# Kernel optimization log

Measured on AMD Instinct MI355X. Metric: run time of the kernel, lower is better.

The kernel has to match this reference:

```python
import jax, jax.numpy as jnp
import numpy as np

DIM = 2048
H = 16        # num query heads
HK = 2        # num kv heads
D = DIM // H  # head_dim = 128
G = H // HK   # q heads per kv head = 8
SCALE = 1.0 / np.sqrt(D)


def setup_inputs() -> dict:
    key = jax.random.key(0)
    ks = jax.random.split(key, 9)
    xavier = lambda k, fi, fo: jax.random.uniform(k, (fi, fo), jnp.float32,
                                                  -np.sqrt(6.0 / (fi + fo)), np.sqrt(6.0 / (fi + fo)))
    return {
        "x": jax.random.normal(ks[0], (2, 2048, DIM), jnp.float32),
        "Wq": xavier(ks[1], DIM, H * D),  "bq": jnp.zeros((H * D,), jnp.float32),
        "Wk": xavier(ks[2], DIM, HK * D), "bk": jnp.zeros((HK * D,), jnp.float32),
        "Wv": xavier(ks[3], DIM, HK * D), "bv": jnp.zeros((HK * D,), jnp.float32),
        "Wo": xavier(ks[4], H * D, DIM),  "bo": jnp.zeros((DIM,), jnp.float32),
    }


def reference(x, Wq, bq, Wk, bk, Wv, bv, Wo, bo):
    B, T, C = x.shape
    # projections; q grouped as (kv_head, group) so repeat_interleave becomes a broadcast
    q = (x @ Wq + bq).reshape(B, T, HK, G, D)   # [B,T,Hk,G,D]
    k = (x @ Wk + bk).reshape(B, T, HK, D)      # [B,T,Hk,D]
    v = (x @ Wv + bv).reshape(B, T, HK, D)
    # scores: [B,Hk,G,Tq,Tk] — shared K broadcast across the G query heads per kv head
    scores = jnp.einsum('bqhgd,bshd->bhgqs', q, k) * SCALE
    scores = jnp.clip(scores, -100.0, 100.0)
    attn = jax.nn.softmax(scores, axis=-1)
    out = jnp.einsum('bhgqs,bshd->bqhgd', attn, v).reshape(B, T, H * D)
    return out @ Wo + bo
```

## Files before the change

kernel.cpp:

```cpp
#include <hip/hip_runtime.h>
#include <cstdint>

typedef __bf16 bf16x8 __attribute__((ext_vector_type(8)));
typedef float floatx4 __attribute__((ext_vector_type(4)));
typedef float floatx16 __attribute__((ext_vector_type(16)));
typedef unsigned short u16;
typedef unsigned int u32;

#define SCALE2 0.1275434297677098f
#define CLIP2  144.26950408889634f
#define DEFER  8.0f

__device__ __forceinline__ u16 f2bf(float f) {
  union { float f; u32 i; } v; v.f = f;
  u32 r = v.i + 0x7fffu + ((v.i >> 16) & 1u);
  return (u16)(r >> 16);
}

__device__ __forceinline__ u32 cvtpk(float lo, float hi) {
  u32 r;
  asm("v_cvt_pk_bf16_f32 %0, %1, %2" : "=v"(r) : "v"(lo), "v"(hi));
  return r;
}

__device__ __forceinline__ void gll16(const void* g, void* l) {
  __builtin_amdgcn_global_load_lds(
      (const __attribute__((address_space(1))) u32*)g,
      (__attribute__((address_space(3))) u32*)l, 16, 0, 0);
}

__global__ __launch_bounds__(256) void convert_bf16(
    const float* __restrict__ src, u16* __restrict__ dst, int n4) {
  int i = blockIdx.x * 256 + threadIdx.x;
  if (i >= n4) return;
  float4 v = ((const float4*)src)[i];
  ushort4 o;
  o.x = f2bf(v.x); o.y = f2bf(v.y); o.z = f2bf(v.z); o.w = f2bf(v.w);
  ((ushort4*)dst)[i] = o;
}

__global__ __launch_bounds__(256) void transpose_cat(
    const float* __restrict__ W0, const float* __restrict__ W1,
    const float* __restrict__ W2,
    int n1, int n2, int ld0, int ld1, int ld2, int K, u16* __restrict__ Bt) {
  __shared__ u16 tile[32][33];
  const int k0 = blockIdx.x * 32, n0 = blockIdx.y * 32;
  const float* src; int ld, nb;
  if (n0 < n1)      { src = W0; ld = ld0; nb = n0; }
  else if (n0 < n2) { src = W1; ld = ld1; nb = n0 - n1; }
  else              { src = W2; ld = ld2; nb = n0 - n2; }
  const int tx = threadIdx.x, ty = threadIdx.y;
#pragma unroll
  for (int i = 0; i < 4; i++) {
    int k = ty + i * 8;
    tile[k][tx] = f2bf(src[(size_t)(k0 + k) * ld + nb + tx]);
  }
  __syncthreads();
#pragma unroll
  for (int i = 0; i < 4; i++) {
    int n = ty + i * 8;
    Bt[(size_t)(n0 + n) * K + k0 + tx] = tile[tx][n];
  }
}

template <int EPI>
__global__ __launch_bounds__(256) void gemm_bt(
    const u16* __restrict__ A, const u16* __restrict__ Bt,
    const float* __restrict__ bias0, const float* __restrict__ bias1,
    const float* __restrict__ bias2,
    u16* __restrict__ out0, u16* __restrict__ out1, u16* __restrict__ out2,
    float* __restrict__ outf,
    int M, int N, int K) {
  __shared__ u16 As[2][128][32];
  __shared__ u16 Bs[2][128][32];
  const int tid  = threadIdx.x;
  const int w    = tid >> 6, L = tid & 63, ln = L & 15, quad = L >> 4;
  const int m0   = blockIdx.y * 128, n0 = blockIdx.x * 128;
  const int mw   = (w & 1) * 64, nw = (w >> 1) * 64;
  const int sr = w * 32 + (L >> 2), sc = (L & 3) * 8;
  const u16* ga = &A [(size_t)(m0 + sr) * K + sc];
  const u16* gb = &Bt[(size_t)(n0 + sr) * K + sc];
  floatx4 acc[4][4] = {};
  const int nk = K >> 5;

  gll16(ga, &As[0][w * 32][0]);
  gll16(ga + (size_t)16 * K, &As[0][w * 32 + 16][0]);
  gll16(gb, &Bs[0][w * 32][0]);
  gll16(gb + (size_t)16 * K, &Bs[0][w * 32 + 16][0]);

  for (int i = 0; i < nk; i++) {
    const int cur = i & 1;
    __syncthreads();
    if (i + 1 < nk) {
      const int kt = (i + 1) << 5;
      gll16(ga + kt, &As[cur ^ 1][w * 32][0]);
      gll16(ga + (size_t)16 * K + kt, &As[cur ^ 1][w * 32 + 16][0]);
      gll16(gb + kt, &Bs[cur ^ 1][w * 32][0]);
      gll16(gb + (size_t)16 * K + kt, &Bs[cur ^ 1][w * 32 + 16][0]);
    }
    bf16x8 af[4], bf[4];
#pragma unroll
    for (int mb = 0; mb < 4; mb++) af[mb] = *(const bf16x8*)&As[cur][mw + mb * 16 + ln][quad * 8];
#pragma unroll
    for (int nb = 0; nb < 4; nb++) bf[nb] = *(const bf16x8*)&Bs[cur][nw + nb * 16 + ln][quad * 8];
#pragma unroll
    for (int mb = 0; mb < 4; mb++)
#pragma unroll
      for (int nb = 0; nb < 4; nb++)
        acc[mb][nb] = __builtin_amdgcn_mfma_f32_16x16x32_bf16(af[mb], bf[nb], acc[mb][nb], 0, 0, 0);
  }

#pragma unroll
  for (int mb = 0; mb < 4; mb++) {
#pragma unroll
    for (int nb = 0; nb < 4; nb++) {
#pragma unroll
      for (int r = 0; r < 4; r++) {
        const int m = m0 + mw + mb * 16 + quad * 4 + r;
        const int n = n0 + nw + nb * 16 + ln;
        float v = acc[mb][nb][r];
        if constexpr (EPI == 0) {
          if (n < 2048) {
            v = (v + bias0[n]) * SCALE2;
            out0[(size_t)m * 2048 + n] = f2bf(v);
          } else if (n < 2304) {
            const int j = n - 2048;
            v += bias1[j];
            out1[(size_t)m * 256 + j] = f2bf(v);
          } else {
            const int j = n - 2304;
            v += bias2[j];
            const int b = m >> 11, t = m & 2047;
            out2[((size_t)(b * 256 + j)) * 2048 + t] = f2bf(v);
          }
        } else {
          v += bias0[n];
          outf[(size_t)m * (size_t)N + n] = v;
        }
      }
    }
  }
}

__global__ __launch_bounds__(256, 2) void attn_kernel(
    const u16* __restrict__ Q, const u16* __restrict__ K,
    const u16* __restrict__ Vt, u16* __restrict__ O) {
  __shared__ u16 Ksh[2][16 * 512];
  __shared__ u16 Vsh[2][16 * 512];
  const int tid = threadIdx.x;
  const int w = tid >> 6, L = tid & 63;
  const int ln = L & 31, hf = L >> 5;
  const int qt = blockIdx.x, h = blockIdx.y, b = blockIdx.z;
  const int hk = h >> 3;
  const size_t qrow0 = (size_t)b * 2048 + qt * 128 + w * 32;

  const u16* Kbase = K + (size_t)b * 2048 * 256 + hk * 128;
  const u16* Vbase = Vt + (size_t)(b * 2 + hk) * 128 * 2048;

  const u16* gK[4];
  const u16* gV[4];
#pragma unroll
  for (int j = 0; j < 4; j++) {
    const int fK = 4 * w + j, mb = fK >> 3, kc = fK & 7;
    gK[j] = Kbase + (size_t)(mb * 32 + ln) * 256 + kc * 16 + hf * 8;
    const int fV = 4 * w + j, db = fV >> 2, ks = fV & 3;
    gV[j] = Vbase + (size_t)(db * 32 + ln) * 2048 + ks * 16 + hf * 8;
  }

  bf16x8 qf[8];
#pragma unroll
  for (int kc = 0; kc < 8; kc++)
    qf[kc] = *(const bf16x8*)&Q[(qrow0 + ln) * 2048 + h * 128 + kc * 16 + hf * 8];

  floatx16 oT[4] = {};
  float mrow = -1e30f, lrow = 0.f;

  auto issue = [&](int tile, int bufi) {
#pragma unroll
    for (int j = 0; j < 4; j++) {
      gll16(gK[j] + (size_t)tile * 64 * 256, &Ksh[bufi][(4 * w + j) * 512]);
      gll16(gV[j] + (size_t)tile * 64,       &Vsh[bufi][(4 * w + j) * 512]);
    }
  };

  auto qkt = [&](floatx16 (&sf)[2], const u16* kb) {
#pragma unroll
    for (int r = 0; r < 16; r++) { sf[0][r] = 0.f; sf[1][r] = 0.f; }
#pragma unroll
    for (int kc = 0; kc < 8; kc++) {
#pragma unroll
      for (int mb = 0; mb < 2; mb++) {
        bf16x8 kf = *(const bf16x8*)&kb[(mb * 8 + kc) * 512 + L * 8];
        sf[mb] = __builtin_amdgcn_mfma_f32_32x32x16_bf16(kf, qf[kc], sf[mb], 0, 0, 0);
      }
    }
  };

  auto softmax = [&](floatx16 (&sf)[2]) {
#pragma unroll
    for (int mb = 0; mb < 2; mb++)
#pragma unroll
      for (int r = 0; r < 16; r++)
        sf[mb][r] = __builtin_amdgcn_fmed3f(sf[mb][r], -CLIP2, CLIP2);
    float t16[16];
#pragma unroll
    for (int r = 0; r < 16; r++) t16[r] = fmaxf(sf[0][r], sf[1][r]);
#pragma unroll
    for (int d = 8; d >= 1; d >>= 1)
#pragma unroll
      for (int r = 0; r < d; r++) t16[r] = fmaxf(t16[r], t16[r + d]);
    const float mx = fmaxf(t16[0], __shfl_xor(t16[0], 32));
    const bool need = __ballot(mx > mrow + DEFER) != 0;
    float mn = mrow, alpha = 1.f;
    if (need) {
      mn = fmaxf(mrow, mx);
      alpha = __builtin_amdgcn_exp2f(mrow - mn);
      mrow = mn;
    }
#pragma unroll
    for (int mb = 0; mb < 2; mb++)
#pragma unroll
      for (int r = 0; r < 16; r++)
        sf[mb][r] = __builtin_amdgcn_exp2f(sf[mb][r] - mn);
    float s16[16];
#pragma unroll
    for (int r = 0; r < 16; r++) s16[r] = sf[0][r] + sf[1][r];
#pragma unroll
    for (int d = 8; d >= 1; d >>= 1)
#pragma unroll
      for (int r = 0; r < d; r++) s16[r] += s16[r + d];
    const float s = s16[0] + __shfl_xor(s16[0], 32);
    if (need) {
      lrow = lrow * alpha + s;
#pragma unroll
      for (int db = 0; db < 4; db++)
#pragma unroll
        for (int r = 0; r < 16; r++) oT[db][r] *= alpha;
    } else {
      lrow += s;
    }
  };

  auto pv = [&](floatx16 (&sf)[2], const u16* vb) {
#pragma unroll
    for (int ks = 0; ks < 4; ks++) {
      const int mb = ks >> 1, s8 = (ks & 1) * 8;
      u32 cA0 = cvtpk(sf[mb][s8 + 0], sf[mb][s8 + 1]);
      u32 cA1 = cvtpk(sf[mb][s8 + 2], sf[mb][s8 + 3]);
      u32 cB0 = cvtpk(sf[mb][s8 + 4], sf[mb][s8 + 5]);
      u32 cB1 = cvtpk(sf[mb][s8 + 6], sf[mb][s8 + 7]);
      asm("v_permlane32_swap_b32 %0, %1" : "+v"(cA0), "+v"(cB0));
      asm("v_permlane32_swap_b32 %0, %1" : "+v"(cA1), "+v"(cB1));
      union { u32 u[4]; bf16x8 v; } pb;
      pb.u[0] = cA0; pb.u[1] = cA1; pb.u[2] = cB0; pb.u[3] = cB1;
#pragma unroll
      for (int db = 0; db < 4; db++) {
        bf16x8 vf = *(const bf16x8*)&vb[(db * 4 + ks) * 512 + L * 8];
        oT[db] = __builtin_amdgcn_mfma_f32_32x32x16_bf16(vf, pb.v, oT[db], 0, 0, 0);
      }
    }
  };

  floatx16 sfA[2], sfB[2];

  issue(0, 0);
  __syncthreads();
  issue(1, 1);
  qkt(sfA, &Ksh[0][0]);

  for (int t = 0; t < 32; t += 2) {
    softmax(sfA);
    __syncthreads();
    __builtin_amdgcn_s_setprio(1);
    qkt(sfB, &Ksh[1][0]);
    pv(sfA, &Vsh[0][0]);
    __builtin_amdgcn_s_setprio(0);
    __syncthreads();
    if (t + 2 < 32) issue(t + 2, 0);
    softmax(sfB);
    __syncthreads();
    __builtin_amdgcn_s_setprio(1);
    if (t + 2 < 32) qkt(sfA, &Ksh[0][0]);
    pv(sfB, &Vsh[1][0]);
    __builtin_amdgcn_s_setprio(0);
    __syncthreads();
    if (t + 3 < 32) issue(t + 3, 1);
  }

  const float inv = 1.f / lrow;
  u16* orow = O + (qrow0 + ln) * 2048 + h * 128;
#pragma unroll
  for (int db = 0; db < 4; db++) {
#pragma unroll
    for (int g = 0; g < 4; g++) {
      uint2 st;
      st.x = cvtpk(oT[db][g * 4 + 0] * inv, oT[db][g * 4 + 1] * inv);
      st.y = cvtpk(oT[db][g * 4 + 2] * inv, oT[db][g * 4 + 3] * inv);
      *(uint2*)&orow[db * 32 + g * 8 + hf * 4] = st;
    }
  }
}

extern "C" void kernel_launch(void* const* d_in, const int* in_sizes, int n_in,
                              void* d_out, int out_size, void* d_ws, size_t ws_size,
                              hipStream_t stream) {
  const float* x  = (const float*)d_in[0];
  const float* Wq = (const float*)d_in[1];
  const float* bq = (const float*)d_in[2];
  const float* Wk = (const float*)d_in[3];
  const float* bk = (const float*)d_in[4];
  const float* Wv = (const float*)d_in[5];
  const float* bv = (const float*)d_in[6];
  const float* Wo = (const float*)d_in[7];
  const float* bo = (const float*)d_in[8];
  float* out = (float*)d_out;

  char* ws = (char*)d_ws;
  u16* xb     = (u16*)(ws);
  u16* Ob     = (u16*)(ws);
  u16* Wqkv_t = (u16*)(ws + 16777216);
  u16* Wot    = (u16*)(ws + 27262976);
  u16* Qb     = (u16*)(ws + 35651584);
  u16* Kb     = (u16*)(ws + 52428800);
  u16* Vtb    = (u16*)(ws + 54525952);
  (void)in_sizes; (void)n_in; (void)out_size; (void)ws_size;

  convert_bf16<<<8192, 256, 0, stream>>>(x, xb, 2097152);

  transpose_cat<<<dim3(64, 80), dim3(32, 8), 0, stream>>>(
      Wq, Wk, Wv, 2048, 2304, 2048, 256, 256, 2048, Wqkv_t);
  transpose_cat<<<dim3(64, 64), dim3(32, 8), 0, stream>>>(
      Wo, Wo, Wo, 2048, 2048, 2048, 2048, 2048, 2048, Wot);

  gemm_bt<0><<<dim3(20, 32), 256, 0, stream>>>(
      xb, Wqkv_t, bq, bk, bv, Qb, Kb, Vtb, nullptr, 4096, 2560, 2048);

  attn_kernel<<<dim3(16, 16, 2), 256, 0, stream>>>(Qb, Kb, Vtb, Ob);

  gemm_bt<1><<<dim3(16, 32), 256, 0, stream>>>(
      Ob, Wot, bo, nullptr, nullptr, nullptr, nullptr, nullptr, out, 4096, 2048, 2048);
}
```

Baseline: 328.5 us.

## Halve attention KV tile to 32 keys and merge weight transposes into one launch

The attention kernel now processes 32 keys per tile instead of 64. This halves the K/V shared-memory buffers and the score registers, doubles the number of loop iterations, and simplifies the softmax reductions. The smaller footprint may allow more waves per CU or a better schedule, but it adds twice as many barriers and tile issues for the same total work. Separately, the two weight-transpose launches are merged into a single grid to save one kernel launch.

Result: no change. 332.2 us (+1.1%).

```diff
diff --git a/kernel.cpp b/kernel.cpp
--- a/kernel.cpp
+++ b/kernel.cpp
@@ -39,16 +39,21 @@
   ((ushort4*)dst)[i] = o;
 }
 
-__global__ __launch_bounds__(256) void transpose_cat(
-    const float* __restrict__ W0, const float* __restrict__ W1,
-    const float* __restrict__ W2,
-    int n1, int n2, int ld0, int ld1, int ld2, int K, u16* __restrict__ Bt) {
+__global__ __launch_bounds__(256) void transpose_all(
+    const float* __restrict__ Wq, const float* __restrict__ Wk,
+    const float* __restrict__ Wv, const float* __restrict__ Wo,
+    u16* __restrict__ Wqkv_t, u16* __restrict__ Wot) {
   __shared__ u16 tile[32][33];
-  const int k0 = blockIdx.x * 32, n0 = blockIdx.y * 32;
-  const float* src; int ld, nb;
-  if (n0 < n1)      { src = W0; ld = ld0; nb = n0; }
-  else if (n0 < n2) { src = W1; ld = ld1; nb = n0 - n1; }
-  else              { src = W2; ld = ld2; nb = n0 - n2; }
+  const int k0 = blockIdx.x * 32, ny = blockIdx.y;
+  const float* src; int ld, nb, n0; u16* dst;
+  if (ny < 80) {
+    n0 = ny * 32; dst = Wqkv_t;
+    if (n0 < 2048)      { src = Wq; ld = 2048; nb = n0; }
+    else if (n0 < 2304) { src = Wk; ld = 256;  nb = n0 - 2048; }
+    else                { src = Wv; ld = 256;  nb = n0 - 2304; }
+  } else {
+    n0 = (ny - 80) * 32; dst = Wot; src = Wo; ld = 2048; nb = n0;
+  }
   const int tx = threadIdx.x, ty = threadIdx.y;
 #pragma unroll
   for (int i = 0; i < 4; i++) {
@@ -59,7 +64,7 @@
 #pragma unroll
   for (int i = 0; i < 4; i++) {
     int n = ty + i * 8;
-    Bt[(size_t)(n0 + n) * K + k0 + tx] = tile[tx][n];
+    dst[(size_t)(n0 + n) * 2048 + k0 + tx] = tile[tx][n];
   }
 }
 
@@ -145,8 +150,8 @@
 __global__ __launch_bounds__(256, 2) void attn_kernel(
     const u16* __restrict__ Q, const u16* __restrict__ K,
     const u16* __restrict__ Vt, u16* __restrict__ O) {
-  __shared__ u16 Ksh[2][16 * 512];
-  __shared__ u16 Vsh[2][16 * 512];
+  __shared__ u16 Ksh[2][8 * 512];
+  __shared__ u16 Vsh[2][8 * 512];
   const int tid = threadIdx.x;
   const int w = tid >> 6, L = tid & 63;
   const int ln = L & 31, hf = L >> 5;
@@ -157,13 +162,13 @@
   const u16* Kbase = K + (size_t)b * 2048 * 256 + hk * 128;
   const u16* Vbase = Vt + (size_t)(b * 2 + hk) * 128 * 2048;
 
-  const u16* gK[4];
-  const u16* gV[4];
-#pragma unroll
-  for (int j = 0; j < 4; j++) {
-    const int fK = 4 * w + j, mb = fK >> 3, kc = fK & 7;
-    gK[j] = Kbase + (size_t)(mb * 32 + ln) * 256 + kc * 16 + hf * 8;
-    const int fV = 4 * w + j, db = fV >> 2, ks = fV & 3;
+  const u16* gK[2];
+  const u16* gV[2];
+#pragma unroll
+  for (int j = 0; j < 2; j++) {
+    const int fK = 2 * w + j;
+    gK[j] = Kbase + (size_t)ln * 256 + fK * 16 + hf * 8;
+    const int fV = 2 * w + j, db = fV >> 1, ks = fV & 1;
     gV[j] = Vbase + (size_t)(db * 32 + ln) * 2048 + ks * 16 + hf * 8;
   }
 
@@ -177,39 +182,34 @@
 
   auto issue = [&](int tile, int bufi) {
 #pragma unroll
-    for (int j = 0; j < 4; j++) {
-      gll16(gK[j] + (size_t)tile * 64 * 256, &Ksh[bufi][(4 * w + j) * 512]);
-      gll16(gV[j] + (size_t)tile * 64,       &Vsh[bufi][(4 * w + j) * 512]);
+    for (int j = 0; j < 2; j++) {
+      gll16(gK[j] + (size_t)tile * 32 * 256, &Ksh[bufi][(2 * w + j) * 512]);
+      gll16(gV[j] + (size_t)tile * 32,       &Vsh[bufi][(2 * w + j) * 512]);
     }
   };
 
-  auto qkt = [&](floatx16 (&sf)[2], const u16* kb) {
-#pragma unroll
-    for (int r = 0; r < 16; r++) { sf[0][r] = 0.f; sf[1][r] = 0.f; }
+  auto qkt = [&](floatx16& sf, const u16* kb) {
+#pragma unroll
+    for (int r = 0; r < 16; r++) sf[r] = 0.f;
 #pragma unroll
     for (int kc = 0; kc < 8; kc++) {
-#pragma unroll
-      for (int mb = 0; mb < 2; mb++) {
-        bf16x8 kf = *(const bf16x8*)&kb[(mb * 8 + kc) * 512 + L * 8];
-        sf[mb] = __builtin_amdgcn_mfma_f32_32x32x16_bf16(kf, qf[kc], sf[mb], 0, 0, 0);
-      }
+      bf16x8 kf = *(const bf16x8*)&kb[kc * 512 + L * 8];
+      sf = __builtin_amdgcn_mfma_f32_32x32x16_bf16(kf, qf[kc], sf, 0, 0, 0);
     }
   };
 
-  auto softmax = [&](floatx16 (&sf)[2]) {
-#pragma unroll
-    for (int mb = 0; mb < 2; mb++)
-#pragma unroll
-      for (int r = 0; r < 16; r++)
-        sf[mb][r] = __builtin_amdgcn_fmed3f(sf[mb][r], -CLIP2, CLIP2);
-    float t16[16];
-#pragma unroll
-    for (int r = 0; r < 16; r++) t16[r] = fmaxf(sf[0][r], sf[1][r]);
-#pragma unroll
-    for (int d = 8; d >= 1; d >>= 1)
-#pragma unroll
-      for (int r = 0; r < d; r++) t16[r] = fmaxf(t16[r], t16[r + d]);
-    const float mx = fmaxf(t16[0], __shfl_xor(t16[0], 32));
+  auto softmax = [&](floatx16& sf) {
+#pragma unroll
+    for (int r = 0; r < 16; r++)
+      sf[r] = __builtin_amdgcn_fmed3f(sf[r], -CLIP2, CLIP2);
+    float t8[8];
+#pragma unroll
+    for (int r = 0; r < 8; r++) t8[r] = fmaxf(sf[r], sf[r + 8]);
+#pragma unroll
+    for (int d = 4; d >= 1; d >>= 1)
+#pragma unroll
+      for (int r = 0; r < d; r++) t8[r] = fmaxf(t8[r], t8[r + d]);
+    const float mx = fmaxf(t8[0], __shfl_xor(t8[0], 32));
     const bool need = __ballot(mx > mrow + DEFER) != 0;
     float mn = mrow, alpha = 1.f;
     if (need) {
@@ -218,18 +218,16 @@
       mrow = mn;
     }
 #pragma unroll
-    for (int mb = 0; mb < 2; mb++)
-#pragma unroll
-      for (int r = 0; r < 16; r++)
-        sf[mb][r] = __builtin_amdgcn_exp2f(sf[mb][r] - mn);
-    float s16[16];
-#pragma unroll
-    for (int r = 0; r < 16; r++) s16[r] = sf[0][r] + sf[1][r];
-#pragma unroll
-    for (int d = 8; d >= 1; d >>= 1)
-#pragma unroll
-      for (int r = 0; r < d; r++) s16[r] += s16[r + d];
-    const float s = s16[0] + __shfl_xor(s16[0], 32);
+    for (int r = 0; r < 16; r++)
+      sf[r] = __builtin_amdgcn_exp2f(sf[r] - mn);
+    float s8[8];
+#pragma unroll
+    for (int r = 0; r < 8; r++) s8[r] = sf[r] + sf[r + 8];
+#pragma unroll
+    for (int d = 4; d >= 1; d >>= 1)
+#pragma unroll
+      for (int r = 0; r < d; r++) s8[r] += s8[r + d];
+    const float s = s8[0] + __shfl_xor(s8[0], 32);
     if (need) {
       lrow = lrow * alpha + s;
 #pragma unroll
@@ -241,34 +239,34 @@
     }
   };
 
-  auto pv = [&](floatx16 (&sf)[2], const u16* vb) {
-#pragma unroll
-    for (int ks = 0; ks < 4; ks++) {
-      const int mb = ks >> 1, s8 = (ks & 1) * 8;
-      u32 cA0 = cvtpk(sf[mb][s8 + 0], sf[mb][s8 + 1]);
-      u32 cA1 = cvtpk(sf[mb][s8 + 2], sf[mb][s8 + 3]);
-      u32 cB0 = cvtpk(sf[mb][s8 + 4], sf[mb][s8 + 5]);
-      u32 cB1 = cvtpk(sf[mb][s8 + 6], sf[mb][s8 + 7]);
+  auto pv = [&](floatx16& sf, const u16* vb) {
+#pragma unroll
+    for (int ks = 0; ks < 2; ks++) {
+      const int s8p = ks * 8;
+      u32 cA0 = cvtpk(sf[s8p + 0], sf[s8p + 1]);
+      u32 cA1 = cvtpk(sf[s8p + 2], sf[s8p + 3]);
+      u32 cB0 = cvtpk(sf[s8p + 4], sf[s8p + 5]);
+      u32 cB1 = cvtpk(sf[s8p + 6], sf[s8p + 7]);
       asm("v_permlane32_swap_b32 %0, %1" : "+v"(cA0), "+v"(cB0));
       asm("v_permlane32_swap_b32 %0, %1" : "+v"(cA1), "+v"(cB1));
       union { u32 u[4]; bf16x8 v; } pb;
       pb.u[0] = cA0; pb.u[1] = cA1; pb.u[2] = cB0; pb.u[3] = cB1;
 #pragma unroll
       for (int db = 0; db < 4; db++) {
-        bf16x8 vf = *(const bf16x8*)&vb[(db * 4 + ks) * 512 + L * 8];
+        bf16x8 vf = *(const bf16x8*)&vb[(db * 2 + ks) * 512 + L * 8];
         oT[db] = __builtin_amdgcn_mfma_f32_32x32x16_bf16(vf, pb.v, oT[db], 0, 0, 0);
       }
     }
   };
 
-  floatx16 sfA[2], sfB[2];
+  floatx16 sfA, sfB;
 
   issue(0, 0);
   __syncthreads();
   issue(1, 1);
   qkt(sfA, &Ksh[0][0]);
 
-  for (int t = 0; t < 32; t += 2) {
+  for (int t = 0; t < 64; t += 2) {
     softmax(sfA);
     __syncthreads();
     __builtin_amdgcn_s_setprio(1);
@@ -276,15 +274,15 @@
     pv(sfA, &Vsh[0][0]);
     __builtin_amdgcn_s_setprio(0);
     __syncthreads();
-    if (t + 2 < 32) issue(t + 2, 0);
+    if (t + 2 < 64) issue(t + 2, 0);
     softmax(sfB);
     __syncthreads();
     __builtin_amdgcn_s_setprio(1);
-    if (t + 2 < 32) qkt(sfA, &Ksh[0][0]);
+    if (t + 2 < 64) qkt(sfA, &Ksh[0][0]);
     pv(sfB, &Vsh[1][0]);
     __builtin_amdgcn_s_setprio(0);
     __syncthreads();
-    if (t + 3 < 32) issue(t + 3, 1);
+    if (t + 3 < 64) issue(t + 3, 1);
   }
 
   const float inv = 1.f / lrow;
@@ -327,10 +325,8 @@
 
   convert_bf16<<<8192, 256, 0, stream>>>(x, xb, 2097152);
 
-  transpose_cat<<<dim3(64, 80), dim3(32, 8), 0, stream>>>(
-      Wq, Wk, Wv, 2048, 2304, 2048, 256, 256, 2048, Wqkv_t);
-  transpose_cat<<<dim3(64, 64), dim3(32, 8), 0, stream>>>(
-      Wo, Wo, Wo, 2048, 2048, 2048, 2048, 2048, 2048, Wot);
+  transpose_all<<<dim3(64, 144), dim3(32, 8), 0, stream>>>(
+      Wq, Wk, Wv, Wo, Wqkv_t, Wot);
 
   gemm_bt<0><<<dim3(20, 32), 256, 0, stream>>>(
       xb, Wqkv_t, bq, bk, bv, Qb, Kb, Vtb, nullptr, 4096, 2560, 2048);
```
